# Kernel tuning notes

Measured on AMD Instinct MI355X. Metric: run time of the kernel, lower is better.

The kernel has to match this reference:

```python
import jax, jax.numpy as jnp
import numpy as np

B, S, E, H, W = 4, 2048, 1024, 16, 128
HD = E // H

def setup_inputs() -> dict:
    key = jax.random.key(0)
    ks = jax.random.split(key, 5)
    scale = 1.0 / np.sqrt(E)
    x = jax.random.normal(ks[0], (B, S, E), dtype=jnp.float32)
    w_in = jax.random.uniform(ks[1], (3 * E, E), dtype=jnp.float32, minval=-scale, maxval=scale)
    b_in = jnp.zeros((3 * E,), dtype=jnp.float32)
    w_out = jax.random.uniform(ks[2], (E, E), dtype=jnp.float32, minval=-scale, maxval=scale)
    b_out = jnp.zeros((E,), dtype=jnp.float32)
    return {"x": x, "w_in": w_in, "b_in": b_in, "w_out": w_out, "b_out": b_out}

def reference(x, w_in, b_in, w_out, b_out):
    b, s, e = x.shape
    # fused QKV projection (torch MultiheadAttention in_proj)
    qkv = x @ w_in.T + b_in                      # [B,S,3E]
    q, k, v = jnp.split(qkv, 3, axis=-1)
    q = q.reshape(b, s, H, HD).transpose(0, 2, 1, 3)  # [B,H,S,HD]
    k = k.reshape(b, s, H, HD).transpose(0, 2, 1, 3)
    v = v.reshape(b, s, H, HD).transpose(0, 2, 1, 3)
    scores = jnp.einsum('bhqd,bhkd->bhqk', q, k) / jnp.sqrt(jnp.asarray(HD, x.dtype))
    # banded causal mask: row i attends to columns [i-W, i]
    i = jnp.arange(s)[:, None]
    j = jnp.arange(s)[None, :]
    allowed = (j <= i) & (j >= i - W)            # [S,S]
    scores = jnp.where(allowed[None, None], scores, jnp.asarray(-1e9, x.dtype))
    attn = jax.nn.softmax(scores, axis=-1)
    out = jnp.einsum('bhqk,bhkd->bhqd', attn, v)  # [B,H,S,HD]
    out = out.transpose(0, 2, 1, 3).reshape(b, s, e)
    return out @ w_out.T + b_out
```

## Files before the change

### kernel.cpp

```cpp
#include <hip/hip_runtime.h>
#include <stdint.h>

#define SLEN 2048
#define EMB  1024
#define NHEAD 16
#define HDIM  64
#define WINSZ 128

typedef __attribute__((ext_vector_type(8))) __bf16 bf16x8;
typedef __attribute__((ext_vector_type(4))) float  f32x4;

__device__ __forceinline__ unsigned short f2bf(float f) {
  union { float f; unsigned int u; } v;
  v.f = f;
  unsigned int r = v.u + 0x7FFFu + ((v.u >> 16) & 1u);
  return (unsigned short)(r >> 16);
}

__device__ __forceinline__ unsigned int pack_bf(float a, float b) {
  union { float f; unsigned int u; } x, y;
  x.f = a; y.f = b;
  return ((y.u + 0x8000u) & 0xFFFF0000u) | ((x.u + 0x8000u) >> 16);
}

__global__ void cvt_f32_bf16(const float* __restrict__ in, unsigned short* __restrict__ out, int n) {
  int i = (blockIdx.x * 256 + threadIdx.x) * 4;
  if (i >= n) return;
  float4 f = *(const float4*)(in + i);
  ushort4 o;
  o.x = f2bf(f.x); o.y = f2bf(f.y); o.z = f2bf(f.z); o.w = f2bf(f.w);
  *(ushort4*)(out + i) = o;
}

#define AS1(p) (const __attribute__((address_space(1))) unsigned int*)((const void*)(p))
#define AS3(p) (__attribute__((address_space(3))) unsigned int*)((void*)(p))

template <int MODE>
__global__ __launch_bounds__(256, 2) void gemm_nt(
    const unsigned short* __restrict__ A,
    const unsigned short* __restrict__ B,
    const float* __restrict__ bias,
    void* __restrict__ Cout,
    unsigned short* __restrict__ vt,
    int M, int N, int K, int ldc)
{
  __shared__ unsigned short As[128 * 64];
  __shared__ unsigned short Bs[128 * 64];
  const int tid  = threadIdx.x;
  const int wave = tid >> 6, lane = tid & 63;
  const int quad = lane >> 4, l16 = lane & 15;
  const int wm = (wave >> 1) * 64, wn = (wave & 1) * 64;
  const long mBase = (long)blockIdx.y * 128;
  const long nBase = (long)blockIdx.x * 128;
  const int lr  = lane >> 3;
  const int lks = ((lane & 7) ^ lr) * 8;
  const int swz = l16 & 7;

  f32x4 acc[4][4];
#pragma unroll
  for (int i = 0; i < 4; ++i)
#pragma unroll
    for (int j = 0; j < 4; ++j)
#pragma unroll
      for (int r = 0; r < 4; ++r) acc[i][j][r] = 0.f;

  for (int k0 = 0; k0 < K; k0 += 64) {
    __syncthreads();
#pragma unroll
    for (int t = 0; t < 4; ++t) {
      const int r0 = (wave * 4 + t) * 8;
      const unsigned short* ga = A + (mBase + r0 + lr) * (long)K + k0 + lks;
      __builtin_amdgcn_global_load_lds(AS1(ga), AS3(As + r0 * 64), 16, 0, 0);
      const unsigned short* gb = B + (nBase + r0 + lr) * (long)K + k0 + lks;
      __builtin_amdgcn_global_load_lds(AS1(gb), AS3(Bs + r0 * 64), 16, 0, 0);
    }
    __syncthreads();

#pragma unroll
    for (int s = 0; s < 2; ++s) {
      bf16x8 aF[4], bF[4];
#pragma unroll
      for (int i = 0; i < 4; ++i)
        aF[i] = *(const bf16x8*)(As + (wm + i * 16 + l16) * 64 + (((s * 4 + quad) ^ swz) * 8));
#pragma unroll
      for (int j = 0; j < 4; ++j)
        bF[j] = *(const bf16x8*)(Bs + (wn + j * 16 + l16) * 64 + (((s * 4 + quad) ^ swz) * 8));
#pragma unroll
      for (int i = 0; i < 4; ++i)
#pragma unroll
        for (int j = 0; j < 4; ++j)
          acc[i][j] = __builtin_amdgcn_mfma_f32_16x16x32_bf16(aF[i], bF[j], acc[i][j], 0, 0, 0);
    }
  }

  if (MODE == 1 && nBase >= 2048) {
#pragma unroll
    for (int j = 0; j < 4; ++j) {
      const int nG = (int)nBase + wn + j * 16 + l16;
      const float bv = bias[nG];
      const int hd = nG - 2048;
      const int hh = hd >> 6, dd = hd & 63;
#pragma unroll
      for (int i = 0; i < 4; ++i)
#pragma unroll
        for (int r = 0; r < 4; ++r) {
          const int mG = (int)mBase + wm + i * 16 + quad * 4 + r;
          const int bb = mG >> 11, ss = mG & 2047;
          vt[(((long)(bb * NHEAD + hh)) * HDIM + dd) * SLEN + ss] = f2bf(acc[i][j][r] + bv);
        }
    }
  } else {
#pragma unroll
    for (int j = 0; j < 4; ++j) {
      const long nG = nBase + wn + j * 16 + l16;
      const float bv = bias[nG];
#pragma unroll
      for (int i = 0; i < 4; ++i)
#pragma unroll
        for (int r = 0; r < 4; ++r) {
          const long mG = mBase + wm + i * 16 + quad * 4 + r;
          const float v = acc[i][j][r] + bv;
          if (MODE == 1) ((unsigned short*)Cout)[mG * ldc + nG] = f2bf(v);
          else           ((float*)Cout)[mG * ldc + nG] = v;
        }
    }
  }
}

__global__ __launch_bounds__(256, 3) void local_attn(
    const unsigned short* __restrict__ qk,
    const unsigned short* __restrict__ vT,
    unsigned short* __restrict__ outw)
{
  const int qb = blockIdx.x;
  const int h  = blockIdx.y;
  const int b  = blockIdx.z;
  const int tid = threadIdx.x;
  const int wave = tid >> 6, lane = tid & 63;
  const int quad = lane >> 4, l16 = lane & 15;

  __shared__ unsigned short Klds[192 * 64];
  __shared__ unsigned short Vlds[64 * 200];

  const int kwin0 = qb * 64 - WINSZ;

  {
    const int kr = lane >> 3, kc = lane & 7;
    const long colOff = 1024 + h * HDIM + ((kc ^ kr) * 8);
#pragma unroll
    for (int t = 0; t < 6; ++t) {
      const int u = wave * 6 + t;
      const int sk = max(kwin0 + u * 8 + kr, 0);
      const unsigned short* g = qk + (long)(b * SLEN + sk) * 2048 + colOff;
      __builtin_amdgcn_global_load_lds(AS1(g), AS3(Klds + u * 512), 16, 0, 0);
    }
  }
  {
    const unsigned short* vbase = vT + ((long)(b * NHEAD + h)) * HDIM * SLEN;
#pragma unroll
    for (int t = 0; t < 8; ++t) {
      const int c = t * 256 + tid;
      const int d = c >> 5, k8 = c & 31;
      if (k8 < 24) {
        const int s0 = max(kwin0 + k8 * 8, 0);
        uint4 v = *(const uint4*)(vbase + (long)d * SLEN + s0);
        *(uint4*)(Vlds + d * 200 + k8 * 8) = v;
      }
    }
  }

  const int q0 = qb * 64 + wave * 16;
  const long qrow = (long)(b * SLEN + q0 + l16) * 2048 + h * HDIM;
  const bf16x8 qB0 = *(const bf16x8*)(qk + qrow + quad * 8);
  const bf16x8 qB1 = *(const bf16x8*)(qk + qrow + 32 + quad * 8);

  __syncthreads();

  const int lbase = (wave * 16) & ~31;
  const int kx = l16 & 7;
  const int a0 = (quad ^ kx) * 8;
  const int a1 = ((4 + quad) ^ kx) * 8;
  f32x4 sc[5][2];
#pragma unroll
  for (int it = 0; it < 5; ++it) {
    const int l0 = lbase + it * 32;
#pragma unroll
    for (int half = 0; half < 2; ++half) {
      const unsigned short* kr_ = Klds + (l0 + half * 16 + l16) * 64;
      const bf16x8 kA0 = *(const bf16x8*)(kr_ + a0);
      const bf16x8 kA1 = *(const bf16x8*)(kr_ + a1);
      f32x4 s;
#pragma unroll
      for (int r = 0; r < 4; ++r) s[r] = 0.f;
      s = __builtin_amdgcn_mfma_f32_16x16x32_bf16(kA0, qB0, s, 0, 0, 0);
      s = __builtin_amdgcn_mfma_f32_16x16x32_bf16(kA1, qB1, s, 0, 0, 0);
      sc[it][half] = s;
    }
  }

  const int qlocal = WINSZ + wave * 16 + l16;
  const int lo = max(wave * 16 + l16, kwin0 < 0 ? -kwin0 : 0);
  const int kb = lbase + quad * 4;
  float m = -3.0e38f;
#pragma unroll
  for (int it = 0; it < 5; ++it)
#pragma unroll
    for (int half = 0; half < 2; ++half)
#pragma unroll
      for (int r = 0; r < 4; ++r) {
        const int kl = kb + it * 32 + half * 16 + r;
        float v = sc[it][half][r] * 0.125f;
        v = (kl >= lo && kl <= qlocal) ? v : -3.0e38f;
        sc[it][half][r] = v;
        m = fmaxf(m, v);
      }
  m = fmaxf(m, __shfl_xor(m, 16, 64));
  m = fmaxf(m, __shfl_xor(m, 32, 64));

  float lsum = 0.f;
#pragma unroll
  for (int it = 0; it < 5; ++it)
#pragma unroll
    for (int half = 0; half < 2; ++half)
#pragma unroll
      for (int r = 0; r < 4; ++r) {
        const float e = __expf(sc[it][half][r] - m);
        sc[it][half][r] = e;
        lsum += e;
      }
  lsum += __shfl_xor(lsum, 16, 64);
  lsum += __shfl_xor(lsum, 32, 64);
  const float invl = 1.0f / lsum;

  f32x4 Oacc[4];
#pragma unroll
  for (int dt = 0; dt < 4; ++dt)
#pragma unroll
    for (int r = 0; r < 4; ++r) Oacc[dt][r] = 0.f;

#pragma unroll
  for (int it = 0; it < 5; ++it) {
    const int l0 = lbase + it * 32;
    const unsigned int u0 = pack_bf(sc[it][0][0], sc[it][0][1]);
    const unsigned int u1 = pack_bf(sc[it][0][2], sc[it][0][3]);
    const unsigned int u2 = pack_bf(sc[it][1][0], sc[it][1][1]);
    const unsigned int u3 = pack_bf(sc[it][1][2], sc[it][1][3]);
    unsigned int breg[4];
#pragma unroll
    for (int r = 0; r < 4; ++r) {
      const int srcl = ((quad & 1) * 2 + (r >> 1)) * 16 + l16;
      const unsigned int ga = __shfl((int)((r & 1) ? u1 : u0), srcl, 64);
      const unsigned int gb = __shfl((int)((r & 1) ? u3 : u2), srcl, 64);
      breg[r] = (quad >> 1) ? gb : ga;
    }
    union { unsigned int u[4]; bf16x8 v; } pB;
    pB.u[0] = breg[0]; pB.u[1] = breg[1]; pB.u[2] = breg[2]; pB.u[3] = breg[3];
#pragma unroll
    for (int dt = 0; dt < 4; ++dt) {
      const bf16x8 vA = *(const bf16x8*)(Vlds + (dt * 16 + l16) * 200 + l0 + quad * 8);
      Oacc[dt] = __builtin_amdgcn_mfma_f32_16x16x32_bf16(vA, pB.v, Oacc[dt], 0, 0, 0);
    }
  }

  const long obase = (long)(b * SLEN + q0 + l16) * EMB + h * HDIM;
#pragma unroll
  for (int dt = 0; dt < 4; ++dt)
#pragma unroll
    for (int r = 0; r < 4; ++r)
      outw[obase + dt * 16 + quad * 4 + r] = f2bf(Oacc[dt][r] * invl);
}

extern "C" void kernel_launch(void* const* d_in, const int* in_sizes, int n_in,
                              void* d_out, int out_size, void* d_ws, size_t ws_size,
                              hipStream_t stream) {
  const float* x     = (const float*)d_in[0];
  const float* w_in  = (const float*)d_in[1];
  const float* b_in  = (const float*)d_in[2];
  const float* w_out = (const float*)d_in[3];
  const float* b_out = (const float*)d_in[4];
  float* out = (float*)d_out;

  char* ws = (char*)d_ws;
  unsigned short* xb    = (unsigned short*)(ws + 0);
  unsigned short* winb  = (unsigned short*)(ws + 16777216);
  unsigned short* woutb = (unsigned short*)(ws + 23068672);
  unsigned short* qkb   = (unsigned short*)(ws + 25165824);
  unsigned short* attn  = (unsigned short*)(ws + 58720256);
  unsigned short* vT    = (unsigned short*)(ws + 75497472);

  const int nx = 8192 * 1024, nwin = 3072 * 1024, nwout = 1024 * 1024;
  cvt_f32_bf16<<<nx / 1024, 256, 0, stream>>>(x, xb, nx);
  cvt_f32_bf16<<<nwin / 1024, 256, 0, stream>>>(w_in, winb, nwin);
  cvt_f32_bf16<<<nwout / 1024, 256, 0, stream>>>(w_out, woutb, nwout);

  gemm_nt<1><<<dim3(3072 / 128, 8192 / 128), 256, 0, stream>>>(
      xb, winb, b_in, (void*)qkb, vT, 8192, 3072, 1024, 2048);

  local_attn<<<dim3(SLEN / 64, NHEAD, 4), 256, 0, stream>>>(qkb, vT, attn);

  gemm_nt<0><<<dim3(1024 / 128, 8192 / 128), 256, 0, stream>>>(
      attn, woutb, b_out, (void*)out, nullptr, 8192, 1024, 1024, 1024);
}
```

Before: 203.8 us.

## Merge conversion launches and read V directly from global in attention

Replaces three f32-to-bf16 conversion launches with a single kernel that writes into the contiguous workspace. In the local attention kernel, V is no longer staged in shared memory; each wave loads its V fragments straight from global memory before the MFMAs, and the LDS saving allows occupancy hint 4. This removes launch overhead and an LDS staging pass plus its store traffic, at the cost of exposed global-load latency in the PV loop and some redundant V reads across waves.

```diff
diff --git a/kernel.cpp b/kernel.cpp
--- a/kernel.cpp
+++ b/kernel.cpp
@@ -23,13 +23,21 @@
   return ((y.u + 0x8000u) & 0xFFFF0000u) | ((x.u + 0x8000u) >> 16);
 }
 
-__global__ void cvt_f32_bf16(const float* __restrict__ in, unsigned short* __restrict__ out, int n) {
-  int i = (blockIdx.x * 256 + threadIdx.x) * 4;
-  if (i >= n) return;
-  float4 f = *(const float4*)(in + i);
+__global__ void cvt_all(const float* __restrict__ x,
+                        const float* __restrict__ wi,
+                        const float* __restrict__ wo,
+                        unsigned short* __restrict__ dst) {
+  const long n0 = 8388608, n1 = n0 + 3145728, n2 = n1 + 1048576;
+  long i = ((long)blockIdx.x * 256 + threadIdx.x) * 4;
+  if (i >= n2) return;
+  const float* src; long off;
+  if (i < n0)      { src = x;  off = i; }
+  else if (i < n1) { src = wi; off = i - n0; }
+  else             { src = wo; off = i - n1; }
+  float4 f = *(const float4*)(src + off);
   ushort4 o;
   o.x = f2bf(f.x); o.y = f2bf(f.y); o.z = f2bf(f.z); o.w = f2bf(f.w);
-  *(ushort4*)(out + i) = o;
+  *(ushort4*)(dst + i) = o;
 }
 
 #define AS1(p) (const __attribute__((address_space(1))) unsigned int*)((const void*)(p))
@@ -127,7 +135,7 @@
   }
 }
 
-__global__ __launch_bounds__(256, 3) void local_attn(
+__global__ __launch_bounds__(256, 4) void local_attn(
     const unsigned short* __restrict__ qk,
     const unsigned short* __restrict__ vT,
     unsigned short* __restrict__ outw)
@@ -140,7 +148,6 @@
   const int quad = lane >> 4, l16 = lane & 15;
 
   __shared__ unsigned short Klds[192 * 64];
-  __shared__ unsigned short Vlds[64 * 200];
 
   const int kwin0 = qb * 64 - WINSZ;
 
@@ -155,24 +162,13 @@
       __builtin_amdgcn_global_load_lds(AS1(g), AS3(Klds + u * 512), 16, 0, 0);
     }
   }
-  {
-    const unsigned short* vbase = vT + ((long)(b * NHEAD + h)) * HDIM * SLEN;
-#pragma unroll
-    for (int t = 0; t < 8; ++t) {
-      const int c = t * 256 + tid;
-      const int d = c >> 5, k8 = c & 31;
-      if (k8 < 24) {
-        const int s0 = max(kwin0 + k8 * 8, 0);
-        uint4 v = *(const uint4*)(vbase + (long)d * SLEN + s0);
-        *(uint4*)(Vlds + d * 200 + k8 * 8) = v;
-      }
-    }
-  }
 
   const int q0 = qb * 64 + wave * 16;
   const long qrow = (long)(b * SLEN + q0 + l16) * 2048 + h * HDIM;
   const bf16x8 qB0 = *(const bf16x8*)(qk + qrow + quad * 8);
   const bf16x8 qB1 = *(const bf16x8*)(qk + qrow + 32 + quad * 8);
+
+  const unsigned short* vbase = vT + ((long)(b * NHEAD + h)) * HDIM * SLEN;
 
   __syncthreads();
 
@@ -255,9 +251,11 @@
     }
     union { unsigned int u[4]; bf16x8 v; } pB;
     pB.u[0] = breg[0]; pB.u[1] = breg[1]; pB.u[2] = breg[2]; pB.u[3] = breg[3];
+
+    const int col = max(kwin0 + l0 + quad * 8, 0);
 #pragma unroll
     for (int dt = 0; dt < 4; ++dt) {
-      const bf16x8 vA = *(const bf16x8*)(Vlds + (dt * 16 + l16) * 200 + l0 + quad * 8);
+      const bf16x8 vA = *(const bf16x8*)(vbase + (long)(dt * 16 + l16) * SLEN + col);
       Oacc[dt] = __builtin_amdgcn_mfma_f32_16x16x32_bf16(vA, pB.v, Oacc[dt], 0, 0, 0);
     }
   }
@@ -288,10 +286,8 @@
   unsigned short* attn  = (unsigned short*)(ws + 58720256);
   unsigned short* vT    = (unsigned short*)(ws + 75497472);
 
-  const int nx = 8192 * 1024, nwin = 3072 * 1024, nwout = 1024 * 1024;
-  cvt_f32_bf16<<<nx / 1024, 256, 0, stream>>>(x, xb, nx);
-  cvt_f32_bf16<<<nwin / 1024, 256, 0, stream>>>(w_in, winb, nwin);
-  cvt_f32_bf16<<<nwout / 1024, 256, 0, stream>>>(w_out, woutb, nwout);
+  const long ncv = 8388608 + 3145728 + 1048576;
+  cvt_all<<<(int)(ncv / 1024), 256, 0, stream>>>(x, w_in, w_out, xb);
 
   gemm_nt<1><<<dim3(3072 / 128, 8192 / 128), 256, 0, stream>>>(
       xb, winb, b_in, (void*)qkb, vT, 8192, 3072, 1024, 2048);
```

Result: slower. 213.6 us (+4.8%).
